# Performance work log

Measured on AMD Instinct MI355X. Metric: run time of the kernel, lower is better.

## Reference

```python
import jax, jax.numpy as jnp
import numpy as np

EPS = 1e-6
NUM_HEADS = 16
ROPE_THETA = 100000.0


def _rope_tables(seq_len, head_dim, theta):
    inv_freq = 1.0 / (theta ** (np.arange(0, head_dim, 2, dtype=np.float32) / head_dim))
    t = np.arange(seq_len, dtype=np.float32)
    freqs = np.outer(t, inv_freq)                      # (S, head_dim//2)
    emb = np.concatenate([freqs, freqs], axis=-1)      # (S, head_dim)
    return jnp.asarray(np.cos(emb))[None], jnp.asarray(np.sin(emb))[None]  # (1,S,D)


def setup_inputs() -> dict:
    key = jax.random.key(0)
    ks = jax.random.split(key, 6)
    B, S, H = 2, 2048, 1024
    head_dim = H // NUM_HEADS
    cos, sin = _rope_tables(S, head_dim, ROPE_THETA)
    scale = 0.02
    return {
        "hidden_states": jax.random.normal(ks[0], (B, S, H), dtype=jnp.float32),
        "cos": cos, "sin": sin,
        "Wq": jax.random.normal(ks[1], (H, H), dtype=jnp.float32) * scale,
        "bq": jnp.zeros((H,), dtype=jnp.float32),
        "Wk": jax.random.normal(ks[2], (H, H), dtype=jnp.float32) * scale,
        "bk": jnp.zeros((H,), dtype=jnp.float32),
        "Wv": jax.random.normal(ks[3], (H, H), dtype=jnp.float32) * scale,
        "bv": jnp.zeros((H,), dtype=jnp.float32),
        "Wo": jax.random.normal(ks[4], (H, H), dtype=jnp.float32) * scale,
        "bo": jnp.zeros((H,), dtype=jnp.float32),
        "rms_weight": jnp.ones((H,), dtype=jnp.float32),
    }


def _rms_norm(x, w):
    var = jnp.mean(x * x, axis=-1, keepdims=True)
    return x * jax.lax.rsqrt(var + EPS) * w


def _rotate_half(x):
    x1, x2 = jnp.split(x, 2, axis=-1)
    return jnp.concatenate([-x2, x1], axis=-1)


def reference(hidden_states, cos, sin, Wq, bq, Wk, bk, Wv, bv, Wo, bo, rms_weight):
    B, S, H = hidden_states.shape
    D = H // NUM_HEADS
    q = hidden_states @ Wq.T + bq
    k = hidden_states @ Wk.T + bk
    v = hidden_states @ Wv.T + bv
    # RMSNorm over full hidden dim BEFORE head split (as in original)
    q = _rms_norm(q, rms_weight)
    k = _rms_norm(k, rms_weight)
    # (B,S,H) -> (B,heads,S,D)
    q = q.reshape(B, S, NUM_HEADS, D).transpose(0, 2, 1, 3)
    k = k.reshape(B, S, NUM_HEADS, D).transpose(0, 2, 1, 3)
    v = v.reshape(B, S, NUM_HEADS, D).transpose(0, 2, 1, 3)
    # RoPE: cos/sin (1,S,D) -> unsqueeze head dim
    c = cos[:, None, :, :]
    s = sin[:, None, :, :]
    q = q * c + _rotate_half(q) * s
    k = k * c + _rotate_half(k) * s
    # attention (faithful: boolean tril mask is ADDED as 0/1, not -inf)
    scale = D ** 0.5
    scores = jnp.einsum("bhqd,bhkd->bhqk", q, k) / scale
    mask = jnp.tril(jnp.ones((S, S), dtype=scores.dtype))  # +1 on causal, +0 elsewhere
    attn = jax.nn.softmax(scores + mask, axis=-1)
    out = jnp.einsum("bhqk,bhkd->bhqd", attn, v)
    out = out.transpose(0, 2, 1, 3).reshape(B, S, H)
    return out @ Wo.T + bo
```

## Files before the change

kernel.cpp:

```cpp
#include <hip/hip_runtime.h>

typedef unsigned short u16;
typedef __attribute__((ext_vector_type(8))) short bf16x8;
typedef __attribute__((ext_vector_type(4))) float f32x4;

#define MFMA16(A,B,C) __builtin_amdgcn_mfma_f32_16x16x32_bf16(A,B,C,0,0,0)

__device__ __forceinline__ u16 f2bf(float f){
  unsigned int u; __builtin_memcpy(&u,&f,4);
  unsigned int r = (u + 0x7fffu + ((u>>16)&1u)) >> 16;
  return (u16)r;
}
__device__ __forceinline__ float bf2f(u16 h){
  unsigned int u = ((unsigned int)h) << 16;
  float f; __builtin_memcpy(&f,&u,4); return f;
}

__device__ __forceinline__ void async_ld16(const void* g, void* l) {
  __builtin_amdgcn_global_load_lds(
      (const __attribute__((address_space(1))) unsigned int*)g,
      (__attribute__((address_space(3))) unsigned int*)l, 16, 0, 0);
}

__global__ __launch_bounds__(256) void cast_all(const float* __restrict__ hs,
    const float* __restrict__ wq, const float* __restrict__ wk,
    const float* __restrict__ wv, const float* __restrict__ wo,
    u16* __restrict__ dst)
{
  unsigned int i = blockIdx.x*256 + threadIdx.x;
  size_t el = (size_t)i * 8;
  const float* src; size_t off;
  if (el < 4194304) { src = hs; off = el; }
  else {
    unsigned int r = (unsigned int)((el - 4194304) >> 20);
    src = (r==0)?wq:(r==1)?wk:(r==2)?wv:wo;
    off = (el - 4194304) & 1048575;
  }
  float4 a = *reinterpret_cast<const float4*>(src+off);
  float4 b = *reinterpret_cast<const float4*>(src+off+4);
  u16 tmp[8] = {f2bf(a.x),f2bf(a.y),f2bf(a.z),f2bf(a.w),
                f2bf(b.x),f2bf(b.y),f2bf(b.z),f2bf(b.w)};
  *reinterpret_cast<uint4*>(dst + el) = *reinterpret_cast<const uint4*>(tmp);
}

template<int MODE>
__global__ __launch_bounds__(256) void gemm_k(const u16* __restrict__ A,
                                              const u16* __restrict__ W,
                                              const float* __restrict__ b0p,
                                              const float* __restrict__ b1p,
                                              const float* __restrict__ b2p,
                                              void* __restrict__ out,
                                              int M, int N, int K)
{
  __shared__ __align__(16) u16 lds_a[128*32];
  __shared__ __align__(16) u16 lds_w[128*32];
  const int t = threadIdx.x;
  const int lane = t & 63, wave = t >> 6;
  const int wm = wave >> 1, wn = wave & 1;
  const int lr = lane & 15, quad = lane >> 4;
  const int n0 = blockIdx.x * 128, m0 = blockIdx.y * 128;
  const int wbase = t & 192;

  const f32x4 fzero = {0.f,0.f,0.f,0.f};
  f32x4 acc[4][4];
  #pragma unroll
  for (int i=0;i<4;++i)
    #pragma unroll
    for (int j=0;j<4;++j) acc[i][j] = fzero;

  for (int k0 = 0; k0 < K; k0 += 32) {
    __syncthreads();
    #pragma unroll
    for (int it=0; it<2; ++it) {
      int idx = it*256 + t;
      int row = idx >> 2, c8 = (idx & 3) * 8;
      int lbase = (it*256 + wbase) * 8;
      async_ld16(&A[(size_t)(m0+row)*K + k0 + c8], &lds_a[lbase]);
      async_ld16(&W[(size_t)(n0+row)*K + k0 + c8], &lds_w[lbase]);
    }
    __syncthreads();
    bf16x8 af[4], bfr[4];
    #pragma unroll
    for (int mt=0; mt<4; ++mt)
      af[mt] = *reinterpret_cast<const bf16x8*>(&lds_a[(wm*64 + mt*16 + lr)*32 + quad*8]);
    #pragma unroll
    for (int nt=0; nt<4; ++nt)
      bfr[nt] = *reinterpret_cast<const bf16x8*>(&lds_w[(wn*64 + nt*16 + lr)*32 + quad*8]);
    #pragma unroll
    for (int mt=0; mt<4; ++mt)
      #pragma unroll
      for (int nt=0; nt<4; ++nt)
        acc[mt][nt] = MFMA16(af[mt], bfr[nt], acc[mt][nt]);
  }

  if (MODE == 0) {
    float* O = reinterpret_cast<float*>(out);
    #pragma unroll
    for (int nt=0; nt<4; ++nt) {
      int n = n0 + wn*64 + nt*16 + lr;
      float bv = b0p[n];
      #pragma unroll
      for (int mt=0; mt<4; ++mt)
        #pragma unroll
        for (int r=0; r<4; ++r) {
          int m = m0 + wm*64 + mt*16 + quad*4 + r;
          O[(size_t)m * N + n] = acc[mt][nt][r] + bv;
        }
    }
  } else {
    int which = n0 >> 10;
    const float* bp = (which==0) ? b0p : (which==1) ? b1p : b2p;
    u16* dst = reinterpret_cast<u16*>(out) + (size_t)which * 4194304;
    #pragma unroll
    for (int nt=0; nt<4; ++nt) {
      int nn = (n0 & 1023) + wn*64 + nt*16 + lr;
      float bv = bp[nn];
      int hh = nn >> 6, d = nn & 63;
      #pragma unroll
      for (int mt=0; mt<4; ++mt)
        #pragma unroll
        for (int r=0; r<4; ++r) {
          int m = m0 + wm*64 + mt*16 + quad*4 + r;
          int b = m >> 11, s = m & 2047;
          dst[((size_t)(b*16 + hh) * 2048 + s) * 64 + d] = f2bf(acc[mt][nt][r] + bv);
        }
    }
  }
}

__global__ __launch_bounds__(256) void rmsrope(u16* __restrict__ qb, u16* __restrict__ kb,
                                               const float* __restrict__ cosb,
                                               const float* __restrict__ sinb,
                                               const float* __restrict__ w)
{
  u16* buf = blockIdx.y ? kb : qb;
  const int bs = blockIdx.x;
  const int b = bs >> 11, s = bs & 2047;
  const int t = threadIdx.x;
  float x1[2], x2[2];
  float ss = 0.f;
  #pragma unroll
  for (int i=0;i<2;++i){
    int p = t + i*256;
    int h = p >> 5, d = p & 31;
    size_t base = ((size_t)(b*16+h)*2048 + s)*64;
    x1[i] = bf2f(buf[base + d]);
    x2[i] = bf2f(buf[base + d + 32]);
    ss += x1[i]*x1[i] + x2[i]*x2[i];
  }
  #pragma unroll
  for (int off=32; off>0; off>>=1) ss += __shfl_xor(ss, off, 64);
  __shared__ float red[4];
  if ((t & 63) == 0) red[t>>6] = ss;
  __syncthreads();
  float tot = red[0]+red[1]+red[2]+red[3];
  float r = rsqrtf(tot * (1.0f/1024.0f) + 1e-6f);
  #pragma unroll
  for (int i=0;i<2;++i){
    int p = t + i*256;
    int h = p >> 5, d = p & 31;
    size_t base = ((size_t)(b*16+h)*2048 + s)*64;
    float w1 = w[h*64+d], w2 = w[h*64+d+32];
    float n1 = x1[i]*r*w1, n2 = x2[i]*r*w2;
    float c1 = cosb[s*64+d],    s1 = sinb[s*64+d];
    float c2 = cosb[s*64+d+32], s2 = sinb[s*64+d+32];
    buf[base+d]    = f2bf(n1*c1 - n2*s1);
    buf[base+d+32] = f2bf(n2*c2 + n1*s2);
  }
}

__global__ __launch_bounds__(256) void vtrans(const u16* __restrict__ v, u16* __restrict__ vt)
{
  __shared__ __align__(16) u16 tile[64*72];
  const int t = threadIdx.x;
  const int sb = blockIdx.x, bh = blockIdx.y;
  const u16* vp = v + (size_t)bh*2048*64 + (size_t)sb*64*64;
  #pragma unroll
  for (int it=0; it<2; ++it) {
    int idx = it*256 + t;
    int srow = idx >> 3, dch = idx & 7;
    uint4 val = *reinterpret_cast<const uint4*>(&vp[(size_t)srow*64 + dch*8]);
    *reinterpret_cast<uint4*>(&tile[srow*72 + ((dch ^ (srow>>3))&7)*8]) = val;
  }
  __syncthreads();
  u16* op = vt + (size_t)bh*64*2048 + sb*64;
  #pragma unroll
  for (int it=0; it<2; ++it) {
    int idx = it*256 + t;
    int drow = idx >> 3, sch = idx & 7;
    u16 tmp[8];
    #pragma unroll
    for (int i=0;i<8;++i) {
      int srow = sch*8 + i;
      tmp[i] = tile[srow*72 + (((drow>>3) ^ sch)&7)*8 + (drow&7)];
    }
    *reinterpret_cast<uint4*>(&op[(size_t)drow*2048 + sch*8]) = *reinterpret_cast<const uint4*>(tmp);
  }
}

__global__ __launch_bounds__(256) void attn(const u16* __restrict__ qh,
                                            const u16* __restrict__ kh,
                                            const u16* __restrict__ vt,
                                            u16* __restrict__ ao)
{
  __shared__ __align__(16) u16 kbuf[64*64];
  __shared__ __align__(16) u16 vbuf[64*64];
  __shared__ __align__(16) u16 pbuf[4*16*72];
  const int t = threadIdx.x;
  const int lane = t & 63, w = t >> 6;
  const int lr = lane & 15, quad = lane >> 4;
  const int qbase = blockIdx.x * 64;
  const int bh = blockIdx.y;
  const int b = bh >> 4, h = bh & 15;
  const size_t hb = (size_t)bh * 2048 * 64;
  const u16* qp = qh + hb;
  const u16* kp = kh + hb;
  const u16* vtp = vt + hb;

  const int qrow_a = qbase + w*16 + lr;
  bf16x8 qf0 = *reinterpret_cast<const bf16x8*>(&qp[(size_t)qrow_a*64 + quad*8]);
  bf16x8 qf1 = *reinterpret_cast<const bf16x8*>(&qp[(size_t)qrow_a*64 + 32 + quad*8]);

  const f32x4 fzero = {0.f,0.f,0.f,0.f};
  f32x4 oacc[4];
  #pragma unroll
  for (int i=0;i<4;++i) oacc[i] = fzero;
  float lsum[4] = {0.f,0.f,0.f,0.f};
  const int qrow_c = qbase + w*16 + quad*4;
  u16* pw = &pbuf[w*16*72];
  const int fr = lr >> 2;

  for (int kt=0; kt<32; ++kt) {
    __syncthreads();
    #pragma unroll
    for (int it=0; it<2; ++it) {
      int idx = it*256 + t;
      int row = idx >> 3, c = idx & 7;
      uint4 kvv = *reinterpret_cast<const uint4*>(&kp[(size_t)(kt*64+row)*64 + c*8]);
      uint4 vvv = *reinterpret_cast<const uint4*>(&vtp[(size_t)row*2048 + kt*64 + c*8]);
      int sw = ((c ^ (row&7))&7)*8;
      *reinterpret_cast<uint4*>(&kbuf[row*64 + sw]) = kvv;
      *reinterpret_cast<uint4*>(&vbuf[row*64 + sw]) = vvv;
    }
    __syncthreads();

    #pragma unroll
    for (int nt=0; nt<4; ++nt) {
      int row = nt*16 + lr, sw = row & 7;
      bf16x8 b0 = *reinterpret_cast<const bf16x8*>(&kbuf[row*64 + ((quad ^ sw)&7)*8]);
      bf16x8 b1 = *reinterpret_cast<const bf16x8*>(&kbuf[row*64 + ((quad ^ sw ^ 4)&7)*8]);
      f32x4 z = fzero;
      z = MFMA16(qf0, b0, z);
      z = MFMA16(qf1, b1, z);
      int key0 = kt*64 + nt*16 + lr;
      #pragma unroll
      for (int r=0; r<4; ++r) {
        float sc = z[r]*0.125f + ((key0 <= qrow_c + r) ? 1.0f : 0.0f);
        float p = __expf(sc);
        lsum[r] += p;
        int qr = quad*4 + r;
        pw[qr*72 + (((nt*2 + (lr>>3)) ^ quad)<<3) + (lr&7)] = f2bf(p);
      }
    }

    bf16x8 pf0 = *reinterpret_cast<const bf16x8*>(&pw[lr*72 + ((quad ^ fr)&7)*8]);
    bf16x8 pf1 = *reinterpret_cast<const bf16x8*>(&pw[lr*72 + ((quad ^ fr ^ 4)&7)*8]);
    #pragma unroll
    for (int nt=0; nt<4; ++nt) {
      int d = nt*16 + lr, sw = d & 7;
      bf16x8 v0 = *reinterpret_cast<const bf16x8*>(&vbuf[d*64 + ((quad ^ sw)&7)*8]);
      bf16x8 v1 = *reinterpret_cast<const bf16x8*>(&vbuf[d*64 + ((quad ^ sw ^ 4)&7)*8]);
      oacc[nt] = MFMA16(pf0, v0, oacc[nt]);
      oacc[nt] = MFMA16(pf1, v1, oacc[nt]);
    }
  }

  #pragma unroll
  for (int r=0; r<4; ++r) {
    #pragma unroll
    for (int off=1; off<16; off<<=1) lsum[r] += __shfl_xor(lsum[r], off, 64);
  }
  #pragma unroll
  for (int r=0; r<4; ++r) {
    float inv = 1.0f / lsum[r];
    int qrow = qrow_c + r;
    size_t rowbase = ((size_t)(b*2048 + qrow))*1024 + h*64;
    #pragma unroll
    for (int nt=0; nt<4; ++nt)
      ao[rowbase + nt*16 + lr] = f2bf(oacc[nt][r] * inv);
  }
}

extern "C" void kernel_launch(void* const* d_in, const int* in_sizes, int n_in,
                              void* d_out, int out_size, void* d_ws, size_t ws_size,
                              hipStream_t stream)
{
  const float* hs   = (const float*)d_in[0];
  const float* cosb = (const float*)d_in[1];
  const float* sinb = (const float*)d_in[2];
  const float* Wq   = (const float*)d_in[3];
  const float* bq   = (const float*)d_in[4];
  const float* Wk   = (const float*)d_in[5];
  const float* bk   = (const float*)d_in[6];
  const float* Wv   = (const float*)d_in[7];
  const float* bv   = (const float*)d_in[8];
  const float* Wo   = (const float*)d_in[9];
  const float* bo   = (const float*)d_in[10];
  const float* rw   = (const float*)d_in[11];

  const size_t NEL = (size_t)4096 * 1024;
  const size_t WEL = (size_t)1024 * 1024;
  u16* hsb = (u16*)d_ws;
  u16* wqb = hsb + NEL;
  u16* wob = wqb + 3*WEL;
  u16* qhb = wob + WEL;
  u16* khb = qhb + NEL;
  u16* vhb = khb + NEL;
  u16* vtb = vhb + NEL;
  u16* aob = hsb;

  cast_all<<<4096, 256, 0, stream>>>(hs, Wq, Wk, Wv, Wo, hsb);
  gemm_k<1><<<dim3(24,32), 256, 0, stream>>>(hsb, wqb, bq, bk, bv, qhb, 4096, 3072, 1024);
  rmsrope<<<dim3(4096,2), 256, 0, stream>>>(qhb, khb, cosb, sinb, rw);
  vtrans<<<dim3(32,32), 256, 0, stream>>>(vhb, vtb);
  attn<<<dim3(32,32), 256, 0, stream>>>(qhb, khb, vtb, aob);
  gemm_k<0><<<dim3(8,32), 256, 0, stream>>>(aob, wob, bo, nullptr, nullptr, d_out, 4096, 1024, 1024);
}
```

Baseline: 253.4 us.

## Write V transposed from QKV GEMM and keep P in registers in attention

The QKV GEMM epilogue now writes V directly in (head, d, s) layout with 8-byte stores, which removes the separate vtrans kernel and its extra global round trip. The attention kernel swaps MFMA operand roles, computing S^T = K·Q^T, so the exponentiated probabilities land in a register layout that feeds the PV MFMA directly. This drops the per-wave LDS pbuf staging and reduces the row-sum reduction to two shuffles. V fragments are now gathered from LDS as two 4-element pieces per MFMA, and output stores are vectorized.

```diff
diff --git a/kernel.cpp b/kernel.cpp
--- a/kernel.cpp
+++ b/kernel.cpp
@@ -2,6 +2,7 @@
 
 typedef unsigned short u16;
 typedef __attribute__((ext_vector_type(8))) short bf16x8;
+typedef __attribute__((ext_vector_type(4))) short bf16x4;
 typedef __attribute__((ext_vector_type(4))) float f32x4;
 
 #define MFMA16(A,B,C) __builtin_amdgcn_mfma_f32_16x16x32_bf16(A,B,C,0,0,0)
@@ -111,19 +112,38 @@
     int which = n0 >> 10;
     const float* bp = (which==0) ? b0p : (which==1) ? b1p : b2p;
     u16* dst = reinterpret_cast<u16*>(out) + (size_t)which * 4194304;
-    #pragma unroll
-    for (int nt=0; nt<4; ++nt) {
-      int nn = (n0 & 1023) + wn*64 + nt*16 + lr;
-      float bv = bp[nn];
-      int hh = nn >> 6, d = nn & 63;
-      #pragma unroll
-      for (int mt=0; mt<4; ++mt)
+    if (which == 2) {
+      #pragma unroll
+      for (int nt=0; nt<4; ++nt) {
+        int nn = (n0 & 1023) + wn*64 + nt*16 + lr;
+        float bv = bp[nn];
+        int hh = nn >> 6, d = nn & 63;
         #pragma unroll
-        for (int r=0; r<4; ++r) {
-          int m = m0 + wm*64 + mt*16 + quad*4 + r;
+        for (int mt=0; mt<4; ++mt) {
+          int m = m0 + wm*64 + mt*16 + quad*4;
           int b = m >> 11, s = m & 2047;
-          dst[((size_t)(b*16 + hh) * 2048 + s) * 64 + d] = f2bf(acc[mt][nt][r] + bv);
+          u16 o[4];
+          #pragma unroll
+          for (int r=0; r<4; ++r) o[r] = f2bf(acc[mt][nt][r] + bv);
+          *reinterpret_cast<uint2*>(&dst[((size_t)(b*16 + hh)*64 + d)*2048 + s]) =
+              *reinterpret_cast<const uint2*>(o);
         }
+      }
+    } else {
+      #pragma unroll
+      for (int nt=0; nt<4; ++nt) {
+        int nn = (n0 & 1023) + wn*64 + nt*16 + lr;
+        float bv = bp[nn];
+        int hh = nn >> 6, d = nn & 63;
+        #pragma unroll
+        for (int mt=0; mt<4; ++mt)
+          #pragma unroll
+          for (int r=0; r<4; ++r) {
+            int m = m0 + wm*64 + mt*16 + quad*4 + r;
+            int b = m >> 11, s = m & 2047;
+            dst[((size_t)(b*16 + hh) * 2048 + s) * 64 + d] = f2bf(acc[mt][nt][r] + bv);
+          }
+      }
     }
   }
 }
@@ -169,35 +189,6 @@
   }
 }
 
-__global__ __launch_bounds__(256) void vtrans(const u16* __restrict__ v, u16* __restrict__ vt)
-{
-  __shared__ __align__(16) u16 tile[64*72];
-  const int t = threadIdx.x;
-  const int sb = blockIdx.x, bh = blockIdx.y;
-  const u16* vp = v + (size_t)bh*2048*64 + (size_t)sb*64*64;
-  #pragma unroll
-  for (int it=0; it<2; ++it) {
-    int idx = it*256 + t;
-    int srow = idx >> 3, dch = idx & 7;
-    uint4 val = *reinterpret_cast<const uint4*>(&vp[(size_t)srow*64 + dch*8]);
-    *reinterpret_cast<uint4*>(&tile[srow*72 + ((dch ^ (srow>>3))&7)*8]) = val;
-  }
-  __syncthreads();
-  u16* op = vt + (size_t)bh*64*2048 + sb*64;
-  #pragma unroll
-  for (int it=0; it<2; ++it) {
-    int idx = it*256 + t;
-    int drow = idx >> 3, sch = idx & 7;
-    u16 tmp[8];
-    #pragma unroll
-    for (int i=0;i<8;++i) {
-      int srow = sch*8 + i;
-      tmp[i] = tile[srow*72 + (((drow>>3) ^ sch)&7)*8 + (drow&7)];
-    }
-    *reinterpret_cast<uint4*>(&op[(size_t)drow*2048 + sch*8]) = *reinterpret_cast<const uint4*>(tmp);
-  }
-}
-
 __global__ __launch_bounds__(256) void attn(const u16* __restrict__ qh,
                                             const u16* __restrict__ kh,
                                             const u16* __restrict__ vt,
@@ -205,7 +196,6 @@
 {
   __shared__ __align__(16) u16 kbuf[64*64];
   __shared__ __align__(16) u16 vbuf[64*64];
-  __shared__ __align__(16) u16 pbuf[4*16*72];
   const int t = threadIdx.x;
   const int lane = t & 63, w = t >> 6;
   const int lr = lane & 15, quad = lane >> 4;
@@ -217,18 +207,15 @@
   const u16* kp = kh + hb;
   const u16* vtp = vt + hb;
 
-  const int qrow_a = qbase + w*16 + lr;
-  bf16x8 qf0 = *reinterpret_cast<const bf16x8*>(&qp[(size_t)qrow_a*64 + quad*8]);
-  bf16x8 qf1 = *reinterpret_cast<const bf16x8*>(&qp[(size_t)qrow_a*64 + 32 + quad*8]);
+  const int q_abs = qbase + w*16 + lr;
+  bf16x8 qf0 = *reinterpret_cast<const bf16x8*>(&qp[(size_t)q_abs*64 + quad*8]);
+  bf16x8 qf1 = *reinterpret_cast<const bf16x8*>(&qp[(size_t)q_abs*64 + 32 + quad*8]);
 
   const f32x4 fzero = {0.f,0.f,0.f,0.f};
   f32x4 oacc[4];
   #pragma unroll
   for (int i=0;i<4;++i) oacc[i] = fzero;
-  float lsum[4] = {0.f,0.f,0.f,0.f};
-  const int qrow_c = qbase + w*16 + quad*4;
-  u16* pw = &pbuf[w*16*72];
-  const int fr = lr >> 2;
+  float lsum = 0.f;
 
   for (int kt=0; kt<32; ++kt) {
     __syncthreads();
@@ -244,50 +231,60 @@
     }
     __syncthreads();
 
-    #pragma unroll
-    for (int nt=0; nt<4; ++nt) {
-      int row = nt*16 + lr, sw = row & 7;
-      bf16x8 b0 = *reinterpret_cast<const bf16x8*>(&kbuf[row*64 + ((quad ^ sw)&7)*8]);
-      bf16x8 b1 = *reinterpret_cast<const bf16x8*>(&kbuf[row*64 + ((quad ^ sw ^ 4)&7)*8]);
-      f32x4 z = fzero;
-      z = MFMA16(qf0, b0, z);
-      z = MFMA16(qf1, b1, z);
-      int key0 = kt*64 + nt*16 + lr;
-      #pragma unroll
-      for (int r=0; r<4; ++r) {
-        float sc = z[r]*0.125f + ((key0 <= qrow_c + r) ? 1.0f : 0.0f);
-        float p = __expf(sc);
-        lsum[r] += p;
-        int qr = quad*4 + r;
-        pw[qr*72 + (((nt*2 + (lr>>3)) ^ quad)<<3) + (lr&7)] = f2bf(p);
+    bf16x8 pfr[2];
+    #pragma unroll
+    for (int u=0; u<2; ++u) {
+      bf16x4 ph[2];
+      #pragma unroll
+      for (int sidx=0; sidx<2; ++sidx) {
+        int ksub = u*2 + sidx;
+        int row = ksub*16 + lr, sw = row & 7;
+        bf16x8 a0 = *reinterpret_cast<const bf16x8*>(&kbuf[row*64 + ((quad ^ sw)&7)*8]);
+        bf16x8 a1 = *reinterpret_cast<const bf16x8*>(&kbuf[row*64 + ((quad ^ sw ^ 4)&7)*8]);
+        f32x4 z = fzero;
+        z = MFMA16(a0, qf0, z);
+        z = MFMA16(a1, qf1, z);
+        int key0 = kt*64 + ksub*16 + quad*4;
+        u16 pp[4];
+        #pragma unroll
+        for (int r=0; r<4; ++r) {
+          float sc = z[r]*0.125f + ((key0 + r <= q_abs) ? 1.0f : 0.0f);
+          float p = __expf(sc);
+          lsum += p;
+          pp[r] = f2bf(p);
+        }
+        __builtin_memcpy(&ph[sidx], pp, 8);
       }
-    }
-
-    bf16x8 pf0 = *reinterpret_cast<const bf16x8*>(&pw[lr*72 + ((quad ^ fr)&7)*8]);
-    bf16x8 pf1 = *reinterpret_cast<const bf16x8*>(&pw[lr*72 + ((quad ^ fr ^ 4)&7)*8]);
-    #pragma unroll
-    for (int nt=0; nt<4; ++nt) {
-      int d = nt*16 + lr, sw = d & 7;
-      bf16x8 v0 = *reinterpret_cast<const bf16x8*>(&vbuf[d*64 + ((quad ^ sw)&7)*8]);
-      bf16x8 v1 = *reinterpret_cast<const bf16x8*>(&vbuf[d*64 + ((quad ^ sw ^ 4)&7)*8]);
-      oacc[nt] = MFMA16(pf0, v0, oacc[nt]);
-      oacc[nt] = MFMA16(pf1, v1, oacc[nt]);
-    }
-  }
-
-  #pragma unroll
-  for (int r=0; r<4; ++r) {
-    #pragma unroll
-    for (int off=1; off<16; off<<=1) lsum[r] += __shfl_xor(lsum[r], off, 64);
-  }
-  #pragma unroll
-  for (int r=0; r<4; ++r) {
-    float inv = 1.0f / lsum[r];
-    int qrow = qrow_c + r;
-    size_t rowbase = ((size_t)(b*2048 + qrow))*1024 + h*64;
-    #pragma unroll
-    for (int nt=0; nt<4; ++nt)
-      ao[rowbase + nt*16 + lr] = f2bf(oacc[nt][r] * inv);
+      pfr[u] = __builtin_shufflevector(ph[0], ph[1], 0,1,2,3,4,5,6,7);
+    }
+
+    #pragma unroll
+    for (int u=0; u<2; ++u) {
+      #pragma unroll
+      for (int dt=0; dt<4; ++dt) {
+        int row = dt*16 + lr, sw = row & 7;
+        int c0 = u*4 + (quad>>1);
+        int io = (quad&1)*4;
+        bf16x4 v0, v1;
+        __builtin_memcpy(&v0, &vbuf[row*64 + ((c0 ^ sw)&7)*8 + io], 8);
+        __builtin_memcpy(&v1, &vbuf[row*64 + (((c0+2) ^ sw)&7)*8 + io], 8);
+        bf16x8 vf = __builtin_shufflevector(v0, v1, 0,1,2,3,4,5,6,7);
+        oacc[dt] = MFMA16(vf, pfr[u], oacc[dt]);
+      }
+    }
+  }
+
+  lsum += __shfl_xor(lsum, 16, 64);
+  lsum += __shfl_xor(lsum, 32, 64);
+  float inv = 1.0f / lsum;
+  size_t rowbase = ((size_t)(b*2048 + q_abs))*1024 + h*64;
+  #pragma unroll
+  for (int dt=0; dt<4; ++dt) {
+    u16 o[4];
+    #pragma unroll
+    for (int r=0; r<4; ++r) o[r] = f2bf(oacc[dt][r] * inv);
+    *reinterpret_cast<uint2*>(&ao[rowbase + dt*16 + quad*4]) =
+        *reinterpret_cast<const uint2*>(o);
   }
 }
 
@@ -315,14 +312,12 @@
   u16* wob = wqb + 3*WEL;
   u16* qhb = wob + WEL;
   u16* khb = qhb + NEL;
-  u16* vhb = khb + NEL;
-  u16* vtb = vhb + NEL;
+  u16* vtb = khb + NEL;
   u16* aob = hsb;
 
   cast_all<<<4096, 256, 0, stream>>>(hs, Wq, Wk, Wv, Wo, hsb);
   gemm_k<1><<<dim3(24,32), 256, 0, stream>>>(hsb, wqb, bq, bk, bv, qhb, 4096, 3072, 1024);
   rmsrope<<<dim3(4096,2), 256, 0, stream>>>(qhb, khb, cosb, sinb, rw);
-  vtrans<<<dim3(32,32), 256, 0, stream>>>(vhb, vtb);
   attn<<<dim3(32,32), 256, 0, stream>>>(qhb, khb, vtb, aob);
   gemm_k<0><<<dim3(8,32), 256, 0, stream>>>(aob, wob, bo, nullptr, nullptr, d_out, 4096, 1024, 1024);
 }
```

New measurement: 250.0 us. About the same (-1.3%).
